# Kernel tuning notes

Measured on AMD Instinct MI355X. Metric: run time of the kernel, lower is better.

## Reference

```python
import jax, jax.numpy as jnp
import numpy as np

B, M, TP2, H, K, S = 64, 1, 1024, 256, 128, 1024
EPS = 2.220446049250313e-16  # numpy.finfo(float).eps


def setup_inputs() -> dict:
    key = jax.random.key(0)
    ks = jax.random.split(key, 12)
    inp = {
        'event': jax.random.randint(ks[0], (B, M, TP2), 0, K + 3),
        'dtime': jax.random.uniform(ks[1], (B, M, TP2), jnp.float32),
        'post': jax.random.uniform(ks[2], (B, M), jnp.float32),
        'duration': jax.random.uniform(ks[3], (B, M), jnp.float32),
        'dtime_sampling': jax.random.uniform(ks[4], (B, M, S), jnp.float32),
        'index_of_hidden_sampling': jax.random.randint(ks[5], (B, M, S), 0, B * M * (TP2 - 1)),
        'mask_sampling': jnp.ones((B, M, S), jnp.float32),
        # learned parameters
        'Emb': jax.random.normal(ks[6], (K + 3, H), jnp.float32) * 0.05,
        'W': jax.random.normal(ks[7], (7 * H, 2 * H), jnp.float32) * (1.0 / np.sqrt(2 * H)),
        'b': jnp.zeros((7 * H,), jnp.float32),
        'Wl': jax.random.normal(ks[8], (K, H), jnp.float32) * (1.0 / np.sqrt(H)),
    }
    return inp


def reference(event, dtime, post, duration, dtime_sampling, index_of_hidden_sampling,
              mask_sampling, Emb, W, b, Wl):
    Bs, Ms, Tp2 = event.shape
    Hd = Emb.shape[1]
    Tp1 = Tp2 - 1
    emb = Emb[event[:, :, :-1]]            # (B,M,T+1,H)
    dts = dtime[:, :, 1:]                  # (B,M,T+1)
    xs = (jnp.moveaxis(emb, 2, 0), jnp.moveaxis(dts, 2, 0))

    def step(carry, x):
        h, c, cbar = carry
        e, dt = x
        z = jnp.concatenate([e, h], axis=-1) @ W.T + b  # (B,M,7H)
        gi, gf, go, gz, gib, gfb, gd = jnp.split(z, 7, axis=-1)
        gi, gf, go = jax.nn.sigmoid(gi), jax.nn.sigmoid(gf), jax.nn.sigmoid(go)
        gib, gfb = jax.nn.sigmoid(gib), jax.nn.sigmoid(gfb)
        zc = jnp.tanh(gz)
        gd = jax.nn.softplus(gd)  # beta = 1
        c_i = gf * c + gi * zc
        cbar_i = gfb * cbar + gib * zc
        h_plus = go * jnp.tanh(c_i)  # decay with dtime = 0
        c_next = cbar_i + (c_i - cbar_i) * jnp.exp(-gd * dt[..., None])
        h_next = go * jnp.tanh(c_next)
        return (h_next, c_next, cbar_i), (c_i, cbar_i, gd, go, h_next)

    init = tuple(jnp.zeros((Bs, Ms, Hd), dtime.dtype) for _ in range(3))
    _, outs = jax.lax.scan(step, init, xs)
    all_c, all_cb, all_gd, all_go, all_h = (jnp.moveaxis(a, 0, 2) for a in outs)  # (B,M,T+1,H)

    # target + mask (getTarget)
    Kn = Wl.shape[0]
    tgt_raw = event[:, :, 1:]
    mask_complete = (tgt_raw < Kn).astype(dtime.dtype)
    tgt = jnp.where(tgt_raw < Kn, tgt_raw, 0)

    # log-intensity at events (getLogLambda)
    lam = jax.nn.softplus(all_h @ Wl.T)                        # (B,M,T+1,K)
    log_lam = jnp.log(lam + EPS)
    log_lam_tgt = jnp.take_along_axis(log_lam, tgt[..., None], axis=3)[..., 0] * mask_complete

    # sampled states (getSampledStates)
    idx = index_of_hidden_sampling.reshape(-1)
    Sn = dtime_sampling.shape[2]
    gather = lambda a: a.reshape(Bs * Ms * Tp1, Hd)[idx].reshape(Bs, Ms, Sn, Hd)
    cs, cbs, gds, gos = gather(all_c), gather(all_cb), gather(all_gd), gather(all_go)
    c_samp = cbs + (cs - cbs) * jnp.exp(-gds * dtime_sampling[..., None])
    hy = gos * jnp.tanh(c_samp)

    # MC integral (getIntegral)
    lam_s = jax.nn.softplus(hy @ Wl.T).sum(3)                  # (B,M,S)
    lam_mean = (lam_s * mask_sampling).sum(2) / mask_sampling.sum(2)
    integral = lam_mean * duration

    # complete log-likelihood per (batch, particle)
    loglik = log_lam_tgt.sum(2) - integral                     # (B,M)
    return loglik
```

## Files before the change

kernel.cpp:

```cpp
#include <hip/hip_runtime.h>
#include <hip/hip_fp16.h>
#include <cstdint>
#include <cstddef>

#define EPSF 2.220446049250313e-16f

#define Bn   64
#define TP2n 1024
#define Tn   1023
#define Hn   256
#define H7n  1792
#define Kn   128
#define NEn  131

typedef _Float16 f16x2 __attribute__((ext_vector_type(2)));
typedef unsigned uintx4 __attribute__((ext_vector_type(4)));

__device__ __forceinline__ f16x2 u2h(unsigned u) { return __builtin_bit_cast(f16x2, u); }
__device__ __forceinline__ f16x2 f2h(float f)    { return __builtin_bit_cast(f16x2, f); }

__device__ __forceinline__ float fdot2f(f16x2 a, f16x2 b, float c) {
#if __has_builtin(__builtin_amdgcn_fdot2)
  return __builtin_amdgcn_fdot2(a, b, c, false);
#else
  return c + (float)a[0] * (float)b[0] + (float)a[1] * (float)b[1];
#endif
}

__device__ __forceinline__ int sdot4f(unsigned a, unsigned b, int c) {
#if __has_builtin(__builtin_amdgcn_sdot4)
  return __builtin_amdgcn_sdot4((int)a, (int)b, c, false);
#else
  int r = c;
#pragma unroll
  for (int i = 0; i < 4; ++i) {
    int av = ((int)(a << (24 - 8 * i))) >> 24;
    int bv = ((int)(b << (24 - 8 * i))) >> 24;
    r += av * bv;
  }
  return r;
#endif
}

__device__ __forceinline__ float sigmf(float x) { return 1.f / (1.f + __expf(-x)); }

__device__ __forceinline__ float tanhfast(float x) {
  float t = __expf(2.f * fabsf(x));
  float r = 1.f - 2.f / (t + 1.f);
  return copysignf(r, x);
}

__device__ __forceinline__ float softplusf(float x) {
  return fmaxf(x, 0.f) + log1pf(__expf(-fabsf(x)));
}

__device__ __host__ __forceinline__ int orig_row(int rp) {
  int role = rp / 448, i = rp % 448;
  return (i >> 6) * 256 + 64 * role + (i & 63);
}

__global__ void k_ew(const float* __restrict__ Emb, const float* __restrict__ W,
                     const float* __restrict__ bvec, float* __restrict__ EW) {
  int e = blockIdx.x;
  __shared__ float es[Hn];
  for (int k = threadIdx.x; k < Hn; k += blockDim.x) es[k] = Emb[e * Hn + k];
  __syncthreads();
  for (int rp = threadIdx.x; rp < H7n; rp += blockDim.x) {
    int r = orig_row(rp);
    const float* wr = W + (size_t)r * (2 * Hn);
    float acc = bvec[r];
#pragma unroll 4
    for (int k = 0; k < Hn; ++k) acc += es[k] * wr[k];
    EW[e * H7n + rp] = acc;
  }
}

__global__ __launch_bounds__(64) void k_wq8(const float* __restrict__ W,
                                            unsigned* __restrict__ wq,
                                            float* __restrict__ sc) {
  const int rp = blockIdx.x;
  const int r  = orig_row(rp);
  const int j  = threadIdx.x;
  const float* wr = W + (size_t)r * 512 + 256;
  float4 wv = *reinterpret_cast<const float4*>(wr + 4 * j);
  float m = fmaxf(fmaxf(fabsf(wv.x), fabsf(wv.y)),
                  fmaxf(fabsf(wv.z), fabsf(wv.w)));
#pragma unroll
  for (int off = 32; off; off >>= 1) m = fmaxf(m, __shfl_xor(m, off));
  float inv = (m > 0.f) ? 127.f / m : 0.f;
  float v[4] = {wv.x, wv.y, wv.z, wv.w};
  unsigned d = 0;
#pragma unroll
  for (int q = 0; q < 4; ++q) {
    float s = fminf(fmaxf(v[q] * inv, -127.f), 127.f);
    unsigned byte = (unsigned)((int)rintf(s)) & 255u;
    d |= byte << (8 * q);
  }
  wq[(size_t)rp * 64 + j] = d;
  if (j == 0) sc[rp] = m / (127.f * 127.f);
}

__global__ void k_init(float* __restrict__ acc, unsigned* __restrict__ hx) {
  int i = threadIdx.x;
  if (i < 192) acc[i] = 0.f;
  for (int k = i; k < Bn * 128; k += 1024) hx[k] = 1u;
}

__global__ __launch_bounds__(448) void k_scan(
    const int* __restrict__ event, const float* __restrict__ dtime,
    const float* __restrict__ EW, const unsigned* __restrict__ wq,
    const float* __restrict__ sc, unsigned* __restrict__ hx,
    uint2* __restrict__ state) {
  const int x = blockIdx.x;
  const int xcd = x & 7, q = x >> 3;
  const int b = xcd * 8 + (q >> 2);
  const int role = q & 3;
  const int tid = threadIdx.x;
  const int row = role * 448 + tid;

  __shared__ float    zbuf[448];
  __shared__ unsigned hds8[64];
  __shared__ int      ev_s[TP2n];
  __shared__ float    dt_s[TP2n];

  const uintx4* wp = reinterpret_cast<const uintx4*>(wq) + (size_t)row * 16;
  const float  sc_r = sc[row];
  unsigned* hxb = hx + (size_t)b * 128;

  for (int i = tid; i < TP2n; i += 448) {
    ev_s[i] = event[b * TP2n + i];
    dt_s[i] = dtime[b * TP2n + i];
  }
  if (tid < 64) hds8[tid] = 0u;
  __syncthreads();

  float c_r = 0.f, cb_r = 0.f;
  const int j_u = 64 * role + tid;
  float ew_pf = EW[(size_t)ev_s[0] * H7n + row];

  for (int t = 0; t < Tn; ++t) {
    float ewc = ew_pf;
    ew_pf = EW[(size_t)ev_s[t + 1] * H7n + row];

    int acc0 = 0, acc1 = 0, acc2 = 0, acc3 = 0;
    const uintx4* h8 = reinterpret_cast<const uintx4*>(hds8);
#pragma unroll
    for (int i = 0; i < 16; ++i) {
      uintx4 ww = wp[i];
      uintx4 hh = h8[i];
      acc0 = sdot4f(ww[0], hh[0], acc0);
      acc1 = sdot4f(ww[1], hh[1], acc1);
      acc2 = sdot4f(ww[2], hh[2], acc2);
      acc3 = sdot4f(ww[3], hh[3], acc3);
    }
    zbuf[tid] = ewc + sc_r * (float)((acc0 + acc1) + (acc2 + acc3));
    __syncthreads();

    const unsigned parQ = (unsigned)(t & 1);
    const unsigned tauQ = (unsigned)((t >> 1) & 1);

    if (tid < 64) {
      float gi  = sigmf(zbuf[tid]);
      float gf  = sigmf(zbuf[64 + tid]);
      float go  = sigmf(zbuf[128 + tid]);
      float zc  = tanhfast(zbuf[192 + tid]);
      float gib = sigmf(zbuf[256 + tid]);
      float gfb = sigmf(zbuf[320 + tid]);
      float gd  = softplusf(zbuf[384 + tid]);
      float dt  = dt_s[t + 1];
      float ci  = gf * c_r + gi * zc;
      float cbi = gfb * cb_r + gib * zc;
      float cn  = cbi + (ci - cbi) * __expf(-gd * dt);
      float hn  = go * tanhfast(cn);
      c_r = cn; cb_r = cbi;
      unsigned bq = (unsigned)((int)rintf(
                        fminf(fmaxf(hn * 127.f, -127.f), 127.f))) & 255u;
      unsigned u0 = __shfl(bq, 4 * (tid & 15));
      unsigned u1 = __shfl(bq, 4 * (tid & 15) + 1);
      unsigned u2 = __shfl(bq, 4 * (tid & 15) + 2);
      unsigned u3 = __shfl(bq, 4 * (tid & 15) + 3);
      if (tid < 16) {
        unsigned d = u0 | (u1 << 8) | (u2 << 16) | (u3 << 24);
        hds8[16 * role + tid] = d;
        if (t < Tn - 1)
          __hip_atomic_store(hxb + parQ * 64 + 16 * role + tid,
                             (d & 0xFFFFFFFEu) | tauQ,
                             __ATOMIC_RELAXED, __HIP_MEMORY_SCOPE_AGENT);
      }
      f16x2 p0; p0[0] = (_Float16)ci; p0[1] = (_Float16)cbi;
      f16x2 p1; p1[0] = (_Float16)gd; p1[1] = (_Float16)go;
      uint2 o;
      o.x = __builtin_bit_cast(unsigned, p0);
      o.y = __builtin_bit_cast(unsigned, p1);
      state[((size_t)b * Tn + t) * Hn + j_u] = o;
    } else if (tid < 112 && t < Tn - 1) {
      int k  = tid - 64;
      int rr = (role + 1 + (k >> 4)) & 3;
      int m  = 16 * rr + (k & 15);
      unsigned v;
      do {
        v = __hip_atomic_load(hxb + parQ * 64 + m, __ATOMIC_RELAXED,
                              __HIP_MEMORY_SCOPE_AGENT);
      } while ((v & 1u) != tauQ);
      hds8[m] = v;
    }
    __syncthreads();
  }
}

__global__ __launch_bounds__(256) void k_post(
    const uint2* __restrict__ state, const int* __restrict__ event,
    const float* __restrict__ dtime, const float* __restrict__ Wl,
    float* __restrict__ loglik_sum) {
  const int wid = blockIdx.x * 4 + (threadIdx.x >> 6);
  const int lane = threadIdx.x & 63;
  const int b = wid / Tn;
  const int t = wid - b * Tn;
  const int tgt = event[b * TP2n + t + 1];
  if (tgt >= Kn) return;
  const float dtv = dtime[b * TP2n + t + 1];
  const uint2* srow = state + (size_t)wid * Hn;
  uint4 sA = *reinterpret_cast<const uint4*>(srow + lane * 4);
  uint4 sB = *reinterpret_cast<const uint4*>(srow + lane * 4 + 2);
  float4 wl = *reinterpret_cast<const float4*>(Wl + tgt * Hn + lane * 4);
  float h[4];
#pragma unroll
  for (int qq = 0; qq < 4; ++qq) {
    unsigned lo = (qq == 0) ? sA.x : (qq == 1) ? sA.z : (qq == 2) ? sB.x : sB.z;
    unsigned hi = (qq == 0) ? sA.y : (qq == 1) ? sA.w : (qq == 2) ? sB.y : sB.w;
    f16x2 p0 = u2h(lo), p1 = u2h(hi);
    float c = p0[0], cb = p0[1], gd = p1[0], go = p1[1];
    float cs = cb + (c - cb) * __expf(-gd * dtv);
    h[qq] = go * tanhfast(cs);
  }
  float d = h[0] * wl.x + h[1] * wl.y + h[2] * wl.z + h[3] * wl.w;
#pragma unroll
  for (int off = 32; off; off >>= 1) d += __shfl_down(d, off);
  if (lane == 0) atomicAdd(&loglik_sum[b], __logf(softplusf(d) + EPSF));
}

__global__ __launch_bounds__(128) void k_samp(
    const uint2* __restrict__ state, const float* __restrict__ Wl,
    const int* __restrict__ sidx, const float* __restrict__ sdt,
    const float* __restrict__ smask,
    float* __restrict__ lam_acc, float* __restrict__ mask_acc) {
  const int blk = blockIdx.x;
  const int b = blk >> 4;
  const int base = (b << 10) + (blk & 15) * 64;
  const int tid = threadIdx.x;

  f16x2 wr[128];
  {
    const float* wrow = Wl + tid * Hn;
#pragma unroll
    for (int i = 0; i < 128; ++i) {
      f16x2 v; v[0] = (_Float16)wrow[2 * i]; v[1] = (_Float16)wrow[2 * i + 1];
      wr[i] = v;
    }
  }
  __shared__ float4 hy4[Hn / 8];
  __shared__ float  red[2];
  float accl = 0.f, accm = 0.f;

  int   row = sidx[base];
  float dtv = sdt[base];
  float mk  = smask[base];
  uint4 st = *reinterpret_cast<const uint4*>(state + (size_t)row * Hn + 2 * tid);

  for (int s = 0; s < 64; ++s) {
    f16x2 p0 = u2h(st.x), p1 = u2h(st.y);
    f16x2 q0 = u2h(st.z), q1 = u2h(st.w);
    float cs0 = (float)p0[1] + ((float)p0[0] - (float)p0[1]) * __expf(-(float)p1[0] * dtv);
    float cs1 = (float)q0[1] + ((float)q0[0] - (float)q0[1]) * __expf(-(float)q1[0] * dtv);
    f16x2 hp;
    hp[0] = (_Float16)((float)p1[1] * tanhfast(cs0));
    hp[1] = (_Float16)((float)q1[1] * tanhfast(cs1));
    reinterpret_cast<unsigned*>(hy4)[tid] = __builtin_bit_cast(unsigned, hp);

    uint4 st_n = st; float dt_n = dtv, mk_n = mk;
    if (s < 63) {
      int sg = base + s + 1;
      int r2 = sidx[sg];
      dt_n = sdt[sg];
      mk_n = smask[sg];
      st_n = *reinterpret_cast<const uint4*>(state + (size_t)r2 * Hn + 2 * tid);
    }
    __syncthreads();

    float d = 0.f;
#pragma unroll
    for (int q = 0; q < 32; ++q) {
      float4 hq = hy4[q];
      d = fdot2f(wr[4 * q + 0], f2h(hq.x), d);
      d = fdot2f(wr[4 * q + 1], f2h(hq.y), d);
      d = fdot2f(wr[4 * q + 2], f2h(hq.z), d);
      d = fdot2f(wr[4 * q + 3], f2h(hq.w), d);
    }
    float lam = softplusf(d);
#pragma unroll
    for (int off = 32; off; off >>= 1) lam += __shfl_down(lam, off);
    if ((tid & 63) == 0) red[tid >> 6] = lam;
    __syncthreads();
    if (tid == 0) {
      accl += (red[0] + red[1]) * mk;
      accm += mk;
    }
    st = st_n; dtv = dt_n; mk = mk_n;
  }
  if (tid == 0) {
    atomicAdd(&lam_acc[b], accl);
    atomicAdd(&mask_acc[b], accm);
  }
}

__global__ void k_final(const float* __restrict__ loglik_sum,
                        const float* __restrict__ lam_acc,
                        const float* __restrict__ mask_acc,
                        const float* __restrict__ duration,
                        float* __restrict__ out) {
  int b = threadIdx.x;
  if (b < Bn) out[b] = loglik_sum[b] - (lam_acc[b] / mask_acc[b]) * duration[b];
}

extern "C" void kernel_launch(void* const* d_in, const int* in_sizes, int n_in,
                              void* d_out, int out_size, void* d_ws, size_t ws_size,
                              hipStream_t stream) {
  const int*   event    = (const int*)d_in[0];
  const float* dtime    = (const float*)d_in[1];
  const float* duration = (const float*)d_in[3];
  const float* sdt      = (const float*)d_in[4];
  const int*   sidx     = (const int*)d_in[5];
  const float* smask    = (const float*)d_in[6];
  const float* Emb      = (const float*)d_in[7];
  const float* W        = (const float*)d_in[8];
  const float* bv       = (const float*)d_in[9];
  const float* Wl       = (const float*)d_in[10];

  char* ws = (char*)d_ws;
  float*    EW         = (float*)(ws + 0);
  unsigned* wq         = (unsigned*)(ws + (1u << 20));
  float*    lam_acc    = (float*)(ws + (2u << 20));
  float*    mask_acc   = lam_acc + 64;
  float*    loglik_sum = lam_acc + 128;
  unsigned* hx         = (unsigned*)(ws + (2u << 20) + 8192);
  float*    sc         = (float*)(ws + (2u << 20) + 49152);
  uint2*    state      = (uint2*)(ws + (4u << 20));

  k_ew<<<dim3(NEn), dim3(256), 0, stream>>>(Emb, W, bv, EW);
  k_wq8<<<dim3(H7n), dim3(64), 0, stream>>>(W, wq, sc);
  k_init<<<dim3(1), dim3(1024), 0, stream>>>(lam_acc, hx);
  k_scan<<<dim3(256), dim3(448), 0, stream>>>(event, dtime, EW, wq, sc, hx,
                                              state);
  k_post<<<dim3(16368), dim3(256), 0, stream>>>(state, event, dtime, Wl,
                                                loglik_sum);
  k_samp<<<dim3(1024), dim3(128), 0, stream>>>(state, Wl, sidx, sdt, smask,
                                               lam_acc, mask_acc);
  k_final<<<dim3(1), dim3(64), 0, stream>>>(loglik_sum, lam_acc, mask_acc,
                                            duration, (float*)d_out);
}
```

Measured before the change: 2.481 ms.

## Quantize recurrent weights to int4, int8 sampling projection, parallelize EW precompute

The recurrent weight matrix is quantized to 4-bit nibbles (scale m/7) and unpacked inside the scan's dot loop, halving the per-step weight bytes each thread loads. The sampling kernel drops its per-thread fp16 register copy of Wl for an int8 transposed copy held in shared memory, and quantizes the sampled hidden state to int8 so it can use sdot4. The embedding-times-W precompute now runs on a 2D grid with wave-level reductions instead of serial per-thread loops. These cuts lower memory traffic and register pressure but add substantial quantization error, especially from 4-bit recurrent weights accumulated over a 1023-step recurrence, which may break accuracy.

```diff
diff --git a/kernel.cpp b/kernel.cpp
--- a/kernel.cpp
+++ b/kernel.cpp
@@ -19,14 +19,6 @@
 __device__ __forceinline__ f16x2 u2h(unsigned u) { return __builtin_bit_cast(f16x2, u); }
 __device__ __forceinline__ f16x2 f2h(float f)    { return __builtin_bit_cast(f16x2, f); }
 
-__device__ __forceinline__ float fdot2f(f16x2 a, f16x2 b, float c) {
-#if __has_builtin(__builtin_amdgcn_fdot2)
-  return __builtin_amdgcn_fdot2(a, b, c, false);
-#else
-  return c + (float)a[0] * (float)b[0] + (float)a[1] * (float)b[1];
-#endif
-}
-
 __device__ __forceinline__ int sdot4f(unsigned a, unsigned b, int c) {
 #if __has_builtin(__builtin_amdgcn_sdot4)
   return __builtin_amdgcn_sdot4((int)a, (int)b, c, false);
@@ -59,23 +51,29 @@
   return (i >> 6) * 256 + 64 * role + (i & 63);
 }
 
-__global__ void k_ew(const float* __restrict__ Emb, const float* __restrict__ W,
-                     const float* __restrict__ bvec, float* __restrict__ EW) {
-  int e = blockIdx.x;
+__global__ __launch_bounds__(256) void k_ew(
+    const float* __restrict__ Emb, const float* __restrict__ W,
+    const float* __restrict__ bvec, float* __restrict__ EW) {
+  const int e = blockIdx.x;
+  const int chunk = blockIdx.y;
+  const int tid = threadIdx.x;
   __shared__ float es[Hn];
-  for (int k = threadIdx.x; k < Hn; k += blockDim.x) es[k] = Emb[e * Hn + k];
+  es[tid] = Emb[e * Hn + tid];
   __syncthreads();
-  for (int rp = threadIdx.x; rp < H7n; rp += blockDim.x) {
+  const int wv = tid >> 6, l = tid & 63;
+  float4 ev = reinterpret_cast<const float4*>(es)[l];
+  for (int i = 0; i < 28; ++i) {
+    int rp = chunk * 112 + wv * 28 + i;
     int r = orig_row(rp);
-    const float* wr = W + (size_t)r * (2 * Hn);
-    float acc = bvec[r];
-#pragma unroll 4
-    for (int k = 0; k < Hn; ++k) acc += es[k] * wr[k];
-    EW[e * H7n + rp] = acc;
-  }
-}
-
-__global__ __launch_bounds__(64) void k_wq8(const float* __restrict__ W,
+    float4 wf = *reinterpret_cast<const float4*>(W + (size_t)r * 512 + 4 * l);
+    float s = wf.x * ev.x + wf.y * ev.y + wf.z * ev.z + wf.w * ev.w;
+#pragma unroll
+    for (int off = 32; off; off >>= 1) s += __shfl_down(s, off);
+    if (l == 0) EW[e * H7n + rp] = bvec[r] + s;
+  }
+}
+
+__global__ __launch_bounds__(64) void k_wq4(const float* __restrict__ W,
                                             unsigned* __restrict__ wq,
                                             float* __restrict__ sc) {
   const int rp = blockIdx.x;
@@ -87,17 +85,46 @@
                   fmaxf(fabsf(wv.z), fabsf(wv.w)));
 #pragma unroll
   for (int off = 32; off; off >>= 1) m = fmaxf(m, __shfl_xor(m, off));
+  float inv = (m > 0.f) ? 7.f / m : 0.f;
+  if (j < 32) {
+    float4 a = *reinterpret_cast<const float4*>(wr + 8 * j);
+    float4 bq = *reinterpret_cast<const float4*>(wr + 8 * j + 4);
+    float av[4] = {a.x, a.y, a.z, a.w};
+    float bv[4] = {bq.x, bq.y, bq.z, bq.w};
+    unsigned d = 0;
+#pragma unroll
+    for (int i = 0; i < 4; ++i) {
+      unsigned qa = (unsigned)((int)rintf(fminf(fmaxf(av[i] * inv, -7.f), 7.f))) & 0xFu;
+      unsigned qb = (unsigned)((int)rintf(fminf(fmaxf(bv[i] * inv, -7.f), 7.f))) & 0xFu;
+      d |= (qa | (qb << 4)) << (8 * i);
+    }
+    wq[(size_t)rp * 32 + j] = d;
+  }
+  if (j == 0) sc[rp] = (m / 7.f) / (16.f * 127.f);
+}
+
+__global__ __launch_bounds__(64) void k_wlq(const float* __restrict__ Wl,
+                                            unsigned* __restrict__ wlq,
+                                            float* __restrict__ scl) {
+  const int r = blockIdx.x;
+  const int j = threadIdx.x;
+  const float* row = Wl + (size_t)r * Hn;
+  float4 v = reinterpret_cast<const float4*>(row)[j];
+  float m = fmaxf(fmaxf(fabsf(v.x), fabsf(v.y)),
+                  fmaxf(fabsf(v.z), fabsf(v.w)));
+#pragma unroll
+  for (int off = 32; off; off >>= 1) m = fmaxf(m, __shfl_xor(m, off));
   float inv = (m > 0.f) ? 127.f / m : 0.f;
-  float v[4] = {wv.x, wv.y, wv.z, wv.w};
+  float vv[4] = {v.x, v.y, v.z, v.w};
   unsigned d = 0;
 #pragma unroll
-  for (int q = 0; q < 4; ++q) {
-    float s = fminf(fmaxf(v[q] * inv, -127.f), 127.f);
-    unsigned byte = (unsigned)((int)rintf(s)) & 255u;
-    d |= byte << (8 * q);
-  }
-  wq[(size_t)rp * 64 + j] = d;
-  if (j == 0) sc[rp] = m / (127.f * 127.f);
+  for (int qi = 0; qi < 4; ++qi) {
+    unsigned byte = (unsigned)((int)rintf(
+        fminf(fmaxf(vv[qi] * inv, -127.f), 127.f))) & 255u;
+    d |= byte << (8 * qi);
+  }
+  wlq[(((size_t)(j >> 2)) * 128 + r) * 4 + (j & 3)] = d;
+  if (j == 0) scl[r] = m / (127.f * 127.f);
 }
 
 __global__ void k_init(float* __restrict__ acc, unsigned* __restrict__ hx) {
@@ -119,11 +146,12 @@
   const int row = role * 448 + tid;
 
   __shared__ float    zbuf[448];
-  __shared__ unsigned hds8[64];
+  __shared__ uintx4   hds8q[16];
   __shared__ int      ev_s[TP2n];
   __shared__ float    dt_s[TP2n];
-
-  const uintx4* wp = reinterpret_cast<const uintx4*>(wq) + (size_t)row * 16;
+  unsigned* hds8 = reinterpret_cast<unsigned*>(hds8q);
+
+  const uintx4* wp = reinterpret_cast<const uintx4*>(wq) + (size_t)row * 8;
   const float  sc_r = sc[row];
   unsigned* hxb = hx + (size_t)b * 128;
 
@@ -143,15 +171,19 @@
     ew_pf = EW[(size_t)ev_s[t + 1] * H7n + row];
 
     int acc0 = 0, acc1 = 0, acc2 = 0, acc3 = 0;
-    const uintx4* h8 = reinterpret_cast<const uintx4*>(hds8);
-#pragma unroll
-    for (int i = 0; i < 16; ++i) {
+#pragma unroll
+    for (int i = 0; i < 8; ++i) {
       uintx4 ww = wp[i];
-      uintx4 hh = h8[i];
-      acc0 = sdot4f(ww[0], hh[0], acc0);
-      acc1 = sdot4f(ww[1], hh[1], acc1);
-      acc2 = sdot4f(ww[2], hh[2], acc2);
-      acc3 = sdot4f(ww[3], hh[3], acc3);
+      uintx4 ha = hds8q[2 * i];
+      uintx4 hb = hds8q[2 * i + 1];
+      acc0 = sdot4f((ww[0] << 4) & 0xF0F0F0F0u, ha[0], acc0);
+      acc1 = sdot4f( ww[0]       & 0xF0F0F0F0u, ha[1], acc1);
+      acc2 = sdot4f((ww[1] << 4) & 0xF0F0F0F0u, ha[2], acc2);
+      acc3 = sdot4f( ww[1]       & 0xF0F0F0F0u, ha[3], acc3);
+      acc0 = sdot4f((ww[2] << 4) & 0xF0F0F0F0u, hb[0], acc0);
+      acc1 = sdot4f( ww[2]       & 0xF0F0F0F0u, hb[1], acc1);
+      acc2 = sdot4f((ww[3] << 4) & 0xF0F0F0F0u, hb[2], acc2);
+      acc3 = sdot4f( ww[3]       & 0xF0F0F0F0u, hb[3], acc3);
     }
     zbuf[tid] = ewc + sc_r * (float)((acc0 + acc1) + (acc2 + acc3));
     __syncthreads();
@@ -240,7 +272,8 @@
 }
 
 __global__ __launch_bounds__(128) void k_samp(
-    const uint2* __restrict__ state, const float* __restrict__ Wl,
+    const uint2* __restrict__ state, const unsigned* __restrict__ wlq,
+    const float* __restrict__ scl,
     const int* __restrict__ sidx, const float* __restrict__ sdt,
     const float* __restrict__ smask,
     float* __restrict__ lam_acc, float* __restrict__ mask_acc) {
@@ -249,33 +282,34 @@
   const int base = (b << 10) + (blk & 15) * 64;
   const int tid = threadIdx.x;
 
-  f16x2 wr[128];
-  {
-    const float* wrow = Wl + tid * Hn;
-#pragma unroll
-    for (int i = 0; i < 128; ++i) {
-      f16x2 v; v[0] = (_Float16)wrow[2 * i]; v[1] = (_Float16)wrow[2 * i + 1];
-      wr[i] = v;
-    }
-  }
-  __shared__ float4 hy4[Hn / 8];
+  __shared__ uintx4 wlt4[2048];
+  __shared__ uintx4 hq4[16];
   __shared__ float  red[2];
+
+  const uintx4* wg = reinterpret_cast<const uintx4*>(wlq);
+  for (int i = tid; i < 2048; i += 128) wlt4[i] = wg[i];
+  const float sc_row = scl[tid];
   float accl = 0.f, accm = 0.f;
 
   int   row = sidx[base];
   float dtv = sdt[base];
   float mk  = smask[base];
   uint4 st = *reinterpret_cast<const uint4*>(state + (size_t)row * Hn + 2 * tid);
+  __syncthreads();
 
   for (int s = 0; s < 64; ++s) {
     f16x2 p0 = u2h(st.x), p1 = u2h(st.y);
     f16x2 q0 = u2h(st.z), q1 = u2h(st.w);
     float cs0 = (float)p0[1] + ((float)p0[0] - (float)p0[1]) * __expf(-(float)p1[0] * dtv);
     float cs1 = (float)q0[1] + ((float)q0[0] - (float)q0[1]) * __expf(-(float)q1[0] * dtv);
-    f16x2 hp;
-    hp[0] = (_Float16)((float)p1[1] * tanhfast(cs0));
-    hp[1] = (_Float16)((float)q1[1] * tanhfast(cs1));
-    reinterpret_cast<unsigned*>(hy4)[tid] = __builtin_bit_cast(unsigned, hp);
+    float h0 = (float)p1[1] * tanhfast(cs0);
+    float h1 = (float)q1[1] * tanhfast(cs1);
+    unsigned i0 = (unsigned)((int)rintf(fminf(fmaxf(h0 * 127.f, -127.f), 127.f))) & 255u;
+    unsigned i1 = (unsigned)((int)rintf(fminf(fmaxf(h1 * 127.f, -127.f), 127.f))) & 255u;
+    unsigned p = i0 | (i1 << 8);
+    unsigned pn = __shfl(p, tid + 1);
+    if (!(tid & 1))
+      reinterpret_cast<unsigned*>(hq4)[tid >> 1] = p | (pn << 16);
 
     uint4 st_n = st; float dt_n = dtv, mk_n = mk;
     if (s < 63) {
@@ -287,16 +321,17 @@
     }
     __syncthreads();
 
-    float d = 0.f;
-#pragma unroll
-    for (int q = 0; q < 32; ++q) {
-      float4 hq = hy4[q];
-      d = fdot2f(wr[4 * q + 0], f2h(hq.x), d);
-      d = fdot2f(wr[4 * q + 1], f2h(hq.y), d);
-      d = fdot2f(wr[4 * q + 2], f2h(hq.z), d);
-      d = fdot2f(wr[4 * q + 3], f2h(hq.w), d);
-    }
-    float lam = softplusf(d);
+    int acc = 0;
+#pragma unroll
+    for (int kg = 0; kg < 16; ++kg) {
+      uintx4 w4 = wlt4[kg * 128 + tid];
+      uintx4 h4 = hq4[kg];
+      acc = sdot4f(w4[0], h4[0], acc);
+      acc = sdot4f(w4[1], h4[1], acc);
+      acc = sdot4f(w4[2], h4[2], acc);
+      acc = sdot4f(w4[3], h4[3], acc);
+    }
+    float lam = softplusf(sc_row * (float)acc);
 #pragma unroll
     for (int off = 32; off; off >>= 1) lam += __shfl_down(lam, off);
     if ((tid & 63) == 0) red[tid >> 6] = lam;
@@ -344,17 +379,20 @@
   float*    loglik_sum = lam_acc + 128;
   unsigned* hx         = (unsigned*)(ws + (2u << 20) + 8192);
   float*    sc         = (float*)(ws + (2u << 20) + 49152);
+  unsigned* wlq        = (unsigned*)(ws + (2u << 20) + 131072);
+  float*    scl        = (float*)(ws + (2u << 20) + 196608);
   uint2*    state      = (uint2*)(ws + (4u << 20));
 
-  k_ew<<<dim3(NEn), dim3(256), 0, stream>>>(Emb, W, bv, EW);
-  k_wq8<<<dim3(H7n), dim3(64), 0, stream>>>(W, wq, sc);
+  k_ew<<<dim3(NEn, 16), dim3(256), 0, stream>>>(Emb, W, bv, EW);
+  k_wq4<<<dim3(H7n), dim3(64), 0, stream>>>(W, wq, sc);
+  k_wlq<<<dim3(Kn), dim3(64), 0, stream>>>(Wl, wlq, scl);
   k_init<<<dim3(1), dim3(1024), 0, stream>>>(lam_acc, hx);
   k_scan<<<dim3(256), dim3(448), 0, stream>>>(event, dtime, EW, wq, sc, hx,
                                               state);
   k_post<<<dim3(16368), dim3(256), 0, stream>>>(state, event, dtime, Wl,
                                                 loglik_sum);
-  k_samp<<<dim3(1024), dim3(128), 0, stream>>>(state, Wl, sidx, sdt, smask,
-                                               lam_acc, mask_acc);
+  k_samp<<<dim3(1024), dim3(128), 0, stream>>>(state, wlq, scl, sidx, sdt,
+                                               smask, lam_acc, mask_acc);
   k_final<<<dim3(1), dim3(64), 0, stream>>>(loglik_sum, lam_acc, mask_acc,
                                             duration, (float*)d_out);
 }
```

Result: no change. 2.518 ms (+1.5%).
